# Kernel tuning notes

Hardware: AMD Instinct MI355X
Metric: run time of the kernel (lower is better)

## Reference

```python
import jax, jax.numpy as jnp
import numpy as np

H = 256          # hidden_size
HH, WW = 4, 4
CONV = HH * WW * H   # 4096, conv_out_size
N = 16           # n_subtasks
S = 32           # subtask_size
B = 256          # batch
T = 128          # timesteps
TOT = N + S + H + S + 1 + 1  # 338, RecurrentState width


def setup_inputs() -> dict:
    key = jax.random.key(0)
    ks = jax.random.split(key, 12)
    w = lambda k, shape: (jax.random.normal(k, shape) * 0.02).astype(jnp.float32)
    obs = jax.random.normal(ks[0], (T, B, CONV), jnp.float32)
    task = jax.random.normal(ks[1], (B, N, S), jnp.float32)
    hx0 = jnp.zeros((B, TOT), jnp.float32).at[:, :N].set(1.0 / N)  # uniform pointer init
    return dict(
        obs=obs, task=task, hx0=hx0,
        W_ih=w(ks[2], (3 * H, H)), W_hh=w(ks[3], (3 * H, H)),
        b_ih=jnp.zeros((3 * H,), jnp.float32), b_hh=jnp.zeros((3 * H,), jnp.float32),
        W_f=w(ks[4], (H, CONV + 2 * S + 1)), b_f=jnp.zeros((H,), jnp.float32),
        W_u=w(ks[5], (1, 2 * H)), b_u=jnp.zeros((1,), jnp.float32),
        W_s=w(ks[6], (3, H)), b_s=jnp.zeros((3,), jnp.float32),
        W_pi=w(ks[7], (N, H + S)), b_pi=jnp.zeros((N,), jnp.float32),
        W_beta=w(ks[8], (2, CONV + S)), b_beta=jnp.zeros((2,), jnp.float32),
    )


def reference(obs, task, hx0, W_ih, W_hh, b_ih, b_hh, W_f, b_f, W_u, b_u,
              W_s, b_s, W_pi, b_pi, W_beta, b_beta):
    M = task  # [B, N, S] subtask memory
    p0 = hx0[:, :N]
    r0 = hx0[:, N:N + S]
    h0 = hx0[:, N + S:N + S + H]
    g0 = hx0[:, N + S + H:N + S + H + S]
    b0 = hx0[:, N + S + H + S:N + S + H + S + 1]
    keys = jax.random.split(jax.random.key(42), T * 2).reshape(T, 2)

    def gru(x, h):  # torch.nn.GRUCell math
        gi = x @ W_ih.T + b_ih
        gh = h @ W_hh.T + b_hh
        ir, iz, inn = jnp.split(gi, 3, axis=-1)
        hr, hz, hn = jnp.split(gh, 3, axis=-1)
        rr = jax.nn.sigmoid(ir + hr)
        z = jax.nn.sigmoid(iz + hz)
        n = jnp.tanh(inn + rr * hn)
        return (1.0 - z) * n + z * h

    def step(carry, xs):
        p, r, h, b = carry[0], carry[1], carry[2], carry[4]
        g = carry[3]
        x, kk = xs
        # s = f(cat(x, r, g, b))
        s = jnp.concatenate([x, r, g, b], axis=-1) @ W_f.T + b_f
        # update gate c = sigmoid(phi_update(cat(s, h)))
        c = jax.nn.sigmoid(jnp.concatenate([s, h], axis=-1) @ W_u.T + b_u)  # [B,1]
        h_new = gru(s, h)
        # pointer shift: l = softmax(phi_shift(h_old)); p = conv1d(p, l) (same-pad, k=3)
        l = jax.nn.softmax(h @ W_s.T + b_s, axis=1)  # [B,3]
        pp = jnp.pad(p, ((0, 0), (1, 1)))
        p_new = l[:, 0:1] * pp[:, :N] + l[:, 1:2] * pp[:, 1:N + 1] + l[:, 2:3] * pp[:, 2:N + 2]
        # memory read r = p @ M
        r_new = jnp.einsum('bn,bns->bs', p_new, M)
        p = c * p_new + (1.0 - c) * p
        r = c * r_new + (1.0 - c) * r
        h = c * h_new + (1.0 - c) * h
        # sample g ~ Cat(pi_theta(h, r)); g embedding = selected memory row
        logits_g = jnp.concatenate([h, r], axis=-1) @ W_pi.T + b_pi  # [B,N]
        g_idx = jax.random.categorical(kk[0], logits_g)  # [B] int
        lp_g = jnp.take_along_axis(jax.nn.log_softmax(logits_g, axis=-1), g_idx[:, None], axis=1)  # [B,1]
        g_vec = jnp.take_along_axis(M, g_idx[:, None, None], axis=1)[:, 0, :]  # [B,S]
        g = c * g_vec + (1.0 - c) * g
        # sample b ~ Cat(beta(x, g))
        logits_b = jnp.concatenate([x, g], axis=-1) @ W_beta.T + b_beta  # [B,2]
        b_idx = jax.random.categorical(kk[1], logits_b)
        lp_b = jnp.take_along_axis(jax.nn.log_softmax(logits_b, axis=-1), b_idx[:, None], axis=1)
        b = b_idx[:, None].astype(jnp.float32)
        log_prob = lp_g + lp_b
        out = jnp.concatenate([p, r, h, g, b, log_prob], axis=-1)  # [B, TOT]
        return (p, r, h, g, b), out

    _, outs = jax.lax.scan(step, (p0, r0, h0, g0, b0), (obs, keys))
    return outs  # [T, B, TOT]
```

## Files before the change

kernel.cpp:

```cpp
#include <hip/hip_runtime.h>


#define RNG_PARTITIONABLE 1

#define T_STEPS 128
#define B_ROWS  256
#define TOT     338
#define CONV    4096
#define LDWF    4161
#define LDWB    4128

typedef float v2f __attribute__((ext_vector_type(2)));

__device__ __forceinline__ void tf2x32(unsigned k0, unsigned k1, unsigned c0, unsigned c1,
                                       unsigned &o0, unsigned &o1) {
  const unsigned ks2 = k0 ^ k1 ^ 0x1BD11BDAu;
  unsigned x0 = c0 + k0;
  unsigned x1 = c1 + k1;
#define TFR(r) { x0 += x1; x1 = (x1 << (r)) | (x1 >> (32 - (r))); x1 ^= x0; }
  TFR(13) TFR(15) TFR(26) TFR(6)
  x0 += k1; x1 += ks2 + 1u;
  TFR(17) TFR(29) TFR(16) TFR(24)
  x0 += ks2; x1 += k0 + 2u;
  TFR(13) TFR(15) TFR(26) TFR(6)
  x0 += k0; x1 += k1 + 3u;
  TFR(17) TFR(29) TFR(16) TFR(24)
  x0 += k1; x1 += ks2 + 4u;
  TFR(13) TFR(15) TFR(26) TFR(6)
  x0 += ks2; x1 += k0 + 5u;
#undef TFR
  o0 = x0; o1 = x1;
}

__device__ __forceinline__ void rng_key(unsigned j, unsigned &k0, unsigned &k1) {
#if RNG_PARTITIONABLE
  tf2x32(0u, 42u, 0u, j, k0, k1);
#else
  unsigned w[2];
  for (int q = 0; q < 2; ++q) {
    unsigned i = 2u*j + (unsigned)q, a, b;
    if (i < 256u) { tf2x32(0u, 42u, i, 256u + i, a, b); w[q] = a; }
    else          { tf2x32(0u, 42u, i - 256u, i, a, b); w[q] = b; }
  }
  k0 = w[0]; k1 = w[1];
#endif
}

__device__ __forceinline__ unsigned rng_bits(unsigned k0, unsigned k1, unsigned idx, unsigned total) {
#if RNG_PARTITIONABLE
  unsigned o0, o1;
  tf2x32(k0, k1, 0u, idx, o0, o1);
  return o0 ^ o1;
#else
  unsigned half = total >> 1, o0, o1;
  if (idx < half) { tf2x32(k0, k1, idx, half + idx, o0, o1); return o0; }
  else            { tf2x32(k0, k1, idx - half, idx, o0, o1); return o1; }
#endif
}

__device__ __forceinline__ float gumbel_from_bits(unsigned bits) {
  float u0 = __uint_as_float(0x3f800000u | (bits >> 9)) - 1.0f;
  float u  = fmaxf(u0, 1.17549435e-38f);
  return -logf(-logf(u));
}

__global__ __launch_bounds__(256) void rng_k(float* __restrict__ ggum, float* __restrict__ bgum) {
  unsigned tid = blockIdx.x * 256u + threadIdx.x;
  const unsigned NG = T_STEPS * B_ROWS * 16;
  const unsigned NB = T_STEPS * B_ROWS * 2;
  if (tid < NG) {
    unsigned t = tid / (B_ROWS * 16);
    unsigned i = tid % (B_ROWS * 16);
    unsigned k0, k1; rng_key(2u * t, k0, k1);
    ggum[tid] = gumbel_from_bits(rng_bits(k0, k1, i, B_ROWS * 16));
  } else if (tid < NG + NB) {
    unsigned q = tid - NG;
    unsigned t = q / (B_ROWS * 2);
    unsigned i = q % (B_ROWS * 2);
    unsigned k0, k1; rng_key(2u * t + 1u, k0, k1);
    bgum[q] = gumbel_from_bits(rng_bits(k0, k1, i, B_ROWS * 2));
  }
}

__global__ __launch_bounds__(768) void prep4_k(const float* __restrict__ W_ih,
                                               const float* __restrict__ W_hh,
                                               float4* __restrict__ WT4) {
  int k2 = blockIdx.x & 127;
  int copy = blockIdx.x >> 7;
  int col = threadIdx.x;
  float a0 = W_ih[(size_t)col * 256 + 2 * k2];
  float a1 = W_ih[(size_t)col * 256 + 2 * k2 + 1];
  float b0 = W_hh[(size_t)col * 256 + 2 * k2];
  float b1 = W_hh[(size_t)col * 256 + 2 * k2 + 1];
  WT4[(size_t)copy * 98304 + (size_t)k2 * 768 + col] = make_float4(a0, b0, a1, b1);
}

__device__ __forceinline__ float waveRed(float v) {
  v += __shfl_down(v, 32, 64);
  v += __shfl_down(v, 16, 64);
  v += __shfl_down(v, 8, 64);
  v += __shfl_down(v, 4, 64);
  v += __shfl_down(v, 2, 64);
  v += __shfl_down(v, 1, 64);
  return v;
}

__global__ __launch_bounds__(256) void bx_k(const float* __restrict__ obs,
                                            const float* __restrict__ W_beta,
                                            const float* __restrict__ b_beta,
                                            float* __restrict__ bxv) {
  int m = blockIdx.x, tid = threadIdx.x;
  const float* row = obs + (size_t)m * CONV;
  float p0 = 0.f, p1 = 0.f;
  for (int i = tid; i < CONV; i += 256) {
    float o = row[i];
    p0 = fmaf(o, W_beta[i], p0);
    p1 = fmaf(o, W_beta[LDWB + i], p1);
  }
  p0 = waveRed(p0); p1 = waveRed(p1);
  __shared__ float sc[2][4];
  int w = tid >> 6;
  if ((tid & 63) == 0) { sc[0][w] = p0; sc[1][w] = p1; }
  __syncthreads();
  if (tid == 0) bxv[(size_t)m * 2 + 0] = sc[0][0] + sc[0][1] + sc[0][2] + sc[0][3] + b_beta[0];
  if (tid == 1) bxv[(size_t)m * 2 + 1] = sc[1][0] + sc[1][1] + sc[1][2] + sc[1][3] + b_beta[1];
}

struct __attribute__((packed, aligned(4))) F4 { float x, y, z, w; };

__global__ __launch_bounds__(256) void gemm1_k(const float* __restrict__ A,
                                               const float* __restrict__ W,
                                               const float* __restrict__ bias,
                                               float* __restrict__ C1) {
  __shared__ __align__(16) float As[32][68];
  __shared__ __align__(16) float Bs[32][68];
  int bid = blockIdx.x;
  int mt = bid & 511, nt = bid >> 9;
  int m0 = mt * 64, n0 = nt * 64;
  int tid = threadIdx.x;
  int tm = tid & 15, tn = tid >> 4;
  int lr = tid >> 2;
  int lc = (tid & 3) * 8;
  v2f acc[4][2];
#pragma unroll
  for (int i = 0; i < 4; ++i) { acc[i][0] = (v2f){0.f, 0.f}; acc[i][1] = (v2f){0.f, 0.f}; }
  for (int k0 = 0; k0 < CONV; k0 += 32) {
    F4 a0 = *(const F4*)(A + (size_t)(m0 + lr) * CONV + k0 + lc);
    F4 a1 = *(const F4*)(A + (size_t)(m0 + lr) * CONV + k0 + lc + 4);
    F4 b0 = *(const F4*)(W + (size_t)(n0 + lr) * LDWF + k0 + lc);
    F4 b1 = *(const F4*)(W + (size_t)(n0 + lr) * LDWF + k0 + lc + 4);
    __syncthreads();
    As[lc + 0][lr] = a0.x; As[lc + 1][lr] = a0.y; As[lc + 2][lr] = a0.z; As[lc + 3][lr] = a0.w;
    As[lc + 4][lr] = a1.x; As[lc + 5][lr] = a1.y; As[lc + 6][lr] = a1.z; As[lc + 7][lr] = a1.w;
    Bs[lc + 0][lr] = b0.x; Bs[lc + 1][lr] = b0.y; Bs[lc + 2][lr] = b0.z; Bs[lc + 3][lr] = b0.w;
    Bs[lc + 4][lr] = b1.x; Bs[lc + 5][lr] = b1.y; Bs[lc + 6][lr] = b1.z; Bs[lc + 7][lr] = b1.w;
    __syncthreads();
#pragma unroll
    for (int kk = 0; kk < 32; ++kk) {
      const float4 av = *(const float4*)&As[kk][tm * 4];
      const float4 bv = *(const float4*)&Bs[kk][tn * 4];
      const v2f bl = (v2f){bv.x, bv.y};
      const v2f bh = (v2f){bv.z, bv.w};
      const float aa[4] = {av.x, av.y, av.z, av.w};
#pragma unroll
      for (int i = 0; i < 4; ++i) {
        v2f ax = (v2f){aa[i], aa[i]};
        acc[i][0] = __builtin_elementwise_fma(ax, bl, acc[i][0]);
        acc[i][1] = __builtin_elementwise_fma(ax, bh, acc[i][1]);
      }
    }
  }
  const int mrow = m0 + tm * 4;
  const int ncol = n0 + tn * 4;
  float4 bv4 = *(const float4*)(bias + ncol);
#pragma unroll
  for (int i = 0; i < 4; ++i) {
    float4 v;
    v.x = acc[i][0].x + bv4.x; v.y = acc[i][0].y + bv4.y;
    v.z = acc[i][1].x + bv4.z; v.w = acc[i][1].y + bv4.w;
    *(float4*)(C1 + (size_t)(mrow + i) * 256 + ncol) = v;
  }
}

__global__ __launch_bounds__(256, 1) void seq_k(
    const float* __restrict__ hx0, const float* __restrict__ task,
    const float* __restrict__ W_f, const float* __restrict__ WT4,
    const float* __restrict__ b_ih, const float* __restrict__ b_hh,
    const float* __restrict__ W_u, const float* __restrict__ b_u,
    const float* __restrict__ W_s, const float* __restrict__ b_s,
    const float* __restrict__ W_pi, const float* __restrict__ b_pi,
    const float* __restrict__ W_beta, const float* __restrict__ C1,
    const float* __restrict__ bxv, const float* __restrict__ ggum,
    const float* __restrict__ bgum, float* __restrict__ out) {
  const int b2 = blockIdx.x;
  const int tid = threadIdx.x;
  const int o = tid;
  const int brow0 = 2 * b2, brow1 = 2 * b2 + 1;
  const float4* __restrict__ wt = (const float4*)WT4 + (size_t)((b2 >> 3) & 1) * 98304;

  __shared__ float wf_sh[65 * 256];
  __shared__ float wpi_sh[288 * 16];
  __shared__ __align__(16) float4 SH4[2][2][128];
  __shared__ float M_sh[2][512];
  __shared__ float red4[2][4][4];
  __shared__ float red16[2][4][16];
  __shared__ float p_sh[2][2][16];
  __shared__ float r_sh[2][2][32];
  __shared__ float g_sh[2][2][32];
  __shared__ float gg_sh[2][16], bg_sh[2][2], bx_sh[2][2];
  __shared__ float wb_sh[2][32], bpi_sh[16];

  for (int i = tid; i < 65 * 256; i += 256) {
    int oo = i / 65, j = i % 65;
    wf_sh[i] = W_f[(size_t)oo * LDWF + CONV + j];
  }
  for (int i = tid; i < 288 * 16; i += 256) wpi_sh[i] = W_pi[i];
  float hold0 = hx0[brow0 * TOT + 48 + o];
  float hold1 = hx0[brow1 * TOT + 48 + o];
  if (tid < 16) {
    p_sh[0][0][tid] = hx0[brow0 * TOT + tid];
    p_sh[1][0][tid] = hx0[brow1 * TOT + tid];
  }
  if (tid < 32) {
    r_sh[0][0][tid] = hx0[brow0 * TOT + 16 + tid];
    r_sh[1][0][tid] = hx0[brow1 * TOT + 16 + tid];
    g_sh[0][0][tid] = hx0[brow0 * TOT + 304 + tid];
    g_sh[1][0][tid] = hx0[brow1 * TOT + 304 + tid];
    wb_sh[0][tid] = W_beta[CONV + tid];
    wb_sh[1][tid] = W_beta[LDWB + CONV + tid];
  }
  if (tid >= 32 && tid < 48) bpi_sh[tid - 32] = b_pi[tid - 32];
  M_sh[0][tid] = task[(size_t)brow0 * 512 + tid];
  M_sh[0][256 + tid] = task[(size_t)brow0 * 512 + 256 + tid];
  M_sh[1][tid] = task[(size_t)brow1 * 512 + tid];
  M_sh[1][256 + tid] = task[(size_t)brow1 * 512 + 256 + tid];
  float bnew0 = hx0[brow0 * TOT + 336];
  float bnew1 = hx0[brow1 * TOT + 336];

  const float bih_r = b_ih[o], bih_z = b_ih[256 + o], bih_n = b_ih[512 + o];
  const float bhh_r = b_hh[o], bhh_z = b_hh[256 + o], bhh_n = b_hh[512 + o];
  const float wu_s = W_u[o], wu_h = W_u[256 + o];
  const float ws0 = W_s[o], ws1 = W_s[256 + o], ws2 = W_s[512 + o];
  const float bu0 = b_u[0], bs0 = b_s[0], bs1 = b_s[1], bs2 = b_s[2];
  __syncthreads();

  float sacc0, sacc1;
  {
    const float* wfr = wf_sh + o * 65;
    sacc0 = C1[(size_t)brow0 * 256 + o];
    sacc1 = C1[(size_t)brow1 * 256 + o];
#pragma unroll
    for (int j = 0; j < 32; ++j) sacc0 = fmaf(r_sh[0][0][j], wfr[j], sacc0);
#pragma unroll
    for (int j = 0; j < 32; ++j) sacc0 = fmaf(g_sh[0][0][j], wfr[32 + j], sacc0);
    sacc0 = fmaf(bnew0, wfr[64], sacc0);
#pragma unroll
    for (int j = 0; j < 32; ++j) sacc1 = fmaf(r_sh[1][0][j], wfr[j], sacc1);
#pragma unroll
    for (int j = 0; j < 32; ++j) sacc1 = fmaf(g_sh[1][0][j], wfr[32 + j], sacc1);
    sacc1 = fmaf(bnew1, wfr[64], sacc1);
    ((float*)&SH4[0][0][o >> 1])[(o & 1) * 2]     = sacc0;
    ((float*)&SH4[0][0][o >> 1])[(o & 1) * 2 + 1] = hold0;
    ((float*)&SH4[0][1][o >> 1])[(o & 1) * 2]     = sacc1;
    ((float*)&SH4[0][1][o >> 1])[(o & 1) * 2 + 1] = hold1;
  }
  {
    float pc0 = fmaf(wu_s, sacc0, wu_h * hold0);
    float q00 = ws0 * hold0, q01 = ws1 * hold0, q02 = ws2 * hold0;
    float pc1 = fmaf(wu_s, sacc1, wu_h * hold1);
    float q10 = ws0 * hold1, q11 = ws1 * hold1, q12 = ws2 * hold1;
    pc0 = waveRed(pc0); q00 = waveRed(q00); q01 = waveRed(q01); q02 = waveRed(q02);
    pc1 = waveRed(pc1); q10 = waveRed(q10); q11 = waveRed(q11); q12 = waveRed(q12);
    int w4 = tid >> 6;
    if ((tid & 63) == 0) {
      red4[0][w4][0] = pc0; red4[0][w4][1] = q00; red4[0][w4][2] = q01; red4[0][w4][3] = q02;
      red4[1][w4][0] = pc1; red4[1][w4][1] = q10; red4[1][w4][2] = q11; red4[1][w4][3] = q12;
    }
  }
  __syncthreads();

  for (int t = 0; t < T_STEPS; ++t) {
    const int pp = t & 1, np = pp ^ 1;

    int tn2 = (t + 1 < T_STEPS) ? t + 1 : t;
    float c1n0 = C1[((size_t)tn2 * 256 + brow0) * 256 + o];
    float c1n1 = C1[((size_t)tn2 * 256 + brow1) * 256 + o];
    if (tid < 32) {
      int rr = tid >> 4, j = tid & 15;
      gg_sh[rr][j] = ggum[((size_t)t * 256 + brow0 + rr) * 16 + j];
    } else if (tid < 36) {
      int q = tid - 32;
      bg_sh[q >> 1][q & 1] = bgum[((size_t)t * 256 + brow0 + (q >> 1)) * 2 + (q & 1)];
    } else if (tid < 40) {
      int q = tid - 36;
      bx_sh[q >> 1][q & 1] = bxv[((size_t)t * 256 + brow0 + (q >> 1)) * 2 + (q & 1)];
    }

    v2f ar0 = (v2f){0.f, 0.f}, az0 = (v2f){0.f, 0.f}, an0 = (v2f){0.f, 0.f};
    v2f ar1 = (v2f){0.f, 0.f}, az1 = (v2f){0.f, 0.f}, an1 = (v2f){0.f, 0.f};
#pragma unroll 4
    for (int k2 = 0; k2 < 128; ++k2) {
      float4 wr = wt[(size_t)(k2 * 3 + 0) * 256 + o];
      float4 wz = wt[(size_t)(k2 * 3 + 1) * 256 + o];
      float4 wn = wt[(size_t)(k2 * 3 + 2) * 256 + o];
      float4 x0 = SH4[pp][0][k2];
      float4 x1 = SH4[pp][1][k2];
      v2f xa0 = (v2f){x0.x, x0.y}, xb0 = (v2f){x0.z, x0.w};
      v2f xa1 = (v2f){x1.x, x1.y}, xb1 = (v2f){x1.z, x1.w};
      ar0 = __builtin_elementwise_fma(xa0, (v2f){wr.x, wr.y}, ar0);
      ar0 = __builtin_elementwise_fma(xb0, (v2f){wr.z, wr.w}, ar0);
      az0 = __builtin_elementwise_fma(xa0, (v2f){wz.x, wz.y}, az0);
      az0 = __builtin_elementwise_fma(xb0, (v2f){wz.z, wz.w}, az0);
      an0 = __builtin_elementwise_fma(xa0, (v2f){wn.x, wn.y}, an0);
      an0 = __builtin_elementwise_fma(xb0, (v2f){wn.z, wn.w}, an0);
      ar1 = __builtin_elementwise_fma(xa1, (v2f){wr.x, wr.y}, ar1);
      ar1 = __builtin_elementwise_fma(xb1, (v2f){wr.z, wr.w}, ar1);
      az1 = __builtin_elementwise_fma(xa1, (v2f){wz.x, wz.y}, az1);
      az1 = __builtin_elementwise_fma(xb1, (v2f){wz.z, wz.w}, az1);
      an1 = __builtin_elementwise_fma(xa1, (v2f){wn.x, wn.y}, an1);
      an1 = __builtin_elementwise_fma(xb1, (v2f){wn.z, wn.w}, an1);
    }

    float c0, c1, l00, l01, l02, l10, l11, l12;
    {
      float cs0 = red4[0][0][0] + red4[0][1][0] + red4[0][2][0] + red4[0][3][0] + bu0;
      c0 = 1.0f / (1.0f + expf(-cs0));
      float x0 = red4[0][0][1] + red4[0][1][1] + red4[0][2][1] + red4[0][3][1] + bs0;
      float x1 = red4[0][0][2] + red4[0][1][2] + red4[0][2][2] + red4[0][3][2] + bs1;
      float x2 = red4[0][0][3] + red4[0][1][3] + red4[0][2][3] + red4[0][3][3] + bs2;
      float m = fmaxf(x0, fmaxf(x1, x2));
      float e0 = expf(x0 - m), e1 = expf(x1 - m), e2 = expf(x2 - m);
      float es = e0 + e1 + e2;
      l00 = e0 / es; l01 = e1 / es; l02 = e2 / es;
      float cs1 = red4[1][0][0] + red4[1][1][0] + red4[1][2][0] + red4[1][3][0] + bu0;
      c1 = 1.0f / (1.0f + expf(-cs1));
      float y0 = red4[1][0][1] + red4[1][1][1] + red4[1][2][1] + red4[1][3][1] + bs0;
      float y1 = red4[1][0][2] + red4[1][1][2] + red4[1][2][2] + red4[1][3][2] + bs1;
      float y2 = red4[1][0][3] + red4[1][1][3] + red4[1][2][3] + red4[1][3][3] + bs2;
      float mm = fmaxf(y0, fmaxf(y1, y2));
      float f0 = expf(y0 - mm), f1 = expf(y1 - mm), f2 = expf(y2 - mm);
      float fs = f0 + f1 + f2;
      l10 = f0 / fs; l11 = f1 / fs; l12 = f2 / fs;
    }
    const float omc0 = 1.0f - c0, omc1 = 1.0f - c1;

    float pn0[16], pn1[16];
#pragma unroll
    for (int i = 0; i < 16; ++i) {
      float pm0 = (i > 0) ? p_sh[0][pp][i - 1] : 0.f;
      float pq0 = (i < 15) ? p_sh[0][pp][i + 1] : 0.f;
      pn0[i] = l00 * pm0 + l01 * p_sh[0][pp][i] + l02 * pq0;
      float pm1 = (i > 0) ? p_sh[1][pp][i - 1] : 0.f;
      float pq1 = (i < 15) ? p_sh[1][pp][i + 1] : 0.f;
      pn1[i] = l10 * pm1 + l11 * p_sh[1][pp][i] + l12 * pq1;
    }
    float hg0, hg1;
    {
      float rr_ = 1.0f / (1.0f + expf(-(ar0.x + bih_r + ar0.y + bhh_r)));
      float zz = 1.0f / (1.0f + expf(-(az0.x + bih_z + az0.y + bhh_z)));
      float nn = tanhf(an0.x + bih_n + rr_ * (an0.y + bhh_n));
      float hnew = (1.0f - zz) * nn + zz * hold0;
      hg0 = c0 * hnew + omc0 * hold0;
      ((float*)&SH4[np][0][o >> 1])[(o & 1) * 2 + 1] = hg0;
      float rr1 = 1.0f / (1.0f + expf(-(ar1.x + bih_r + ar1.y + bhh_r)));
      float zz1 = 1.0f / (1.0f + expf(-(az1.x + bih_z + az1.y + bhh_z)));
      float nn1 = tanhf(an1.x + bih_n + rr1 * (an1.y + bhh_n));
      float hnew1 = (1.0f - zz1) * nn1 + zz1 * hold1;
      hg1 = c1 * hnew1 + omc1 * hold1;
      ((float*)&SH4[np][1][o >> 1])[(o & 1) * 2 + 1] = hg1;
    }
    float rv0 = 0.f, rv1 = 0.f;
    if (tid < 32) {
      float a0 = 0.f, a1 = 0.f;
#pragma unroll
      for (int n2 = 0; n2 < 16; ++n2) a0 = fmaf(pn0[n2], M_sh[0][n2 * 32 + o], a0);
#pragma unroll
      for (int n2 = 0; n2 < 16; ++n2) a1 = fmaf(pn1[n2], M_sh[1][n2 * 32 + o], a1);
      rv0 = c0 * a0 + omc0 * r_sh[0][pp][o];
      rv1 = c1 * a1 + omc1 * r_sh[1][pp][o];
      r_sh[0][np][o] = rv0;
      r_sh[1][np][o] = rv1;
    }
    if (tid < 16) {
      p_sh[0][np][o] = c0 * pn0[o] + omc0 * p_sh[0][pp][o];
      p_sh[1][np][o] = c1 * pn1[o] + omc1 * p_sh[1][pp][o];
    }
    {
      float pv0[16], pv1[16];
#pragma unroll
      for (int o2 = 0; o2 < 16; ++o2) {
        pv0[o2] = hg0 * wpi_sh[o2 * 288 + o];
        pv1[o2] = hg1 * wpi_sh[o2 * 288 + o];
      }
      if (tid < 32) {
#pragma unroll
        for (int o2 = 0; o2 < 16; ++o2) {
          pv0[o2] = fmaf(rv0, wpi_sh[o2 * 288 + 256 + o], pv0[o2]);
          pv1[o2] = fmaf(rv1, wpi_sh[o2 * 288 + 256 + o], pv1[o2]);
        }
      }
#pragma unroll
      for (int o2 = 0; o2 < 16; ++o2) { pv0[o2] = waveRed(pv0[o2]); pv1[o2] = waveRed(pv1[o2]); }
      int w4 = tid >> 6;
      if ((tid & 63) == 0) {
#pragma unroll
        for (int o2 = 0; o2 < 16; ++o2) { red16[0][w4][o2] = pv0[o2]; red16[1][w4][o2] = pv1[o2]; }
      }
    }
    hold0 = hg0; hold1 = hg1;
    __syncthreads();

    int gidx0 = 0, gidx1 = 0;
    float lpg0, lpg1;
    {
      float lg[16];
#pragma unroll
      for (int n2 = 0; n2 < 16; ++n2)
        lg[n2] = red16[0][0][n2] + red16[0][1][n2] + red16[0][2][n2] + red16[0][3][n2] + bpi_sh[n2];
      float best = -3.402823466e+38f;
      for (int n2 = 0; n2 < 16; ++n2) {
        float v = lg[n2] + gg_sh[0][n2];
        if (v > best) { best = v; gidx0 = n2; }
      }
      float mx = lg[0];
      for (int n2 = 1; n2 < 16; ++n2) mx = fmaxf(mx, lg[n2]);
      float se = 0.f;
      for (int n2 = 0; n2 < 16; ++n2) se += expf(lg[n2] - mx);
      lpg0 = lg[gidx0] - mx - logf(se);
      float best1 = -3.402823466e+38f;
#pragma unroll
      for (int n2 = 0; n2 < 16; ++n2)
        lg[n2] = red16[1][0][n2] + red16[1][1][n2] + red16[1][2][n2] + red16[1][3][n2] + bpi_sh[n2];
      for (int n2 = 0; n2 < 16; ++n2) {
        float v = lg[n2] + gg_sh[1][n2];
        if (v > best1) { best1 = v; gidx1 = n2; }
      }
      float mx1 = lg[0];
      for (int n2 = 1; n2 < 16; ++n2) mx1 = fmaxf(mx1, lg[n2]);
      float se1 = 0.f;
      for (int n2 = 0; n2 < 16; ++n2) se1 += expf(lg[n2] - mx1);
      lpg1 = lg[gidx1] - mx1 - logf(se1);
    }
    if (tid < 32) {
      g_sh[0][np][o] = c0 * M_sh[0][gidx0 * 32 + o] + omc0 * g_sh[0][pp][o];
      g_sh[1][np][o] = c1 * M_sh[1][gidx1 * 32 + o] + omc1 * g_sh[1][pp][o];
    }
    float lpt0, lpt1;
    {
      float lb0 = bx_sh[0][0], lb1 = bx_sh[0][1];
      for (int s2 = 0; s2 < 32; ++s2) {
        float gv = c0 * M_sh[0][gidx0 * 32 + s2] + omc0 * g_sh[0][pp][s2];
        lb0 = fmaf(gv, wb_sh[0][s2], lb0);
        lb1 = fmaf(gv, wb_sh[1][s2], lb1);
      }
      int bidx = ((lb1 + bg_sh[0][1]) > (lb0 + bg_sh[0][0])) ? 1 : 0;
      float mb = fmaxf(lb0, lb1);
      float seb = expf(lb0 - mb) + expf(lb1 - mb);
      bnew0 = (float)bidx;
      lpt0 = lpg0 + ((bidx ? lb1 : lb0) - mb - logf(seb));
      float mb1_0 = bx_sh[1][0], mb1_1 = bx_sh[1][1];
      for (int s2 = 0; s2 < 32; ++s2) {
        float gv = c1 * M_sh[1][gidx1 * 32 + s2] + omc1 * g_sh[1][pp][s2];
        mb1_0 = fmaf(gv, wb_sh[0][s2], mb1_0);
        mb1_1 = fmaf(gv, wb_sh[1][s2], mb1_1);
      }
      int bidx1 = ((mb1_1 + bg_sh[1][1]) > (mb1_0 + bg_sh[1][0])) ? 1 : 0;
      float mbm = fmaxf(mb1_0, mb1_1);
      float seb1 = expf(mb1_0 - mbm) + expf(mb1_1 - mbm);
      bnew1 = (float)bidx1;
      lpt1 = lpg1 + ((bidx1 ? mb1_1 : mb1_0) - mbm - logf(seb1));
    }
    {
      const float* wfr = wf_sh + o * 65;
      sacc0 = c1n0;
#pragma unroll
      for (int j = 0; j < 32; ++j) sacc0 = fmaf(r_sh[0][np][j], wfr[j], sacc0);
#pragma unroll
      for (int j = 0; j < 32; ++j) {
        float gv = c0 * M_sh[0][gidx0 * 32 + j] + omc0 * g_sh[0][pp][j];
        sacc0 = fmaf(gv, wfr[32 + j], sacc0);
      }
      sacc0 = fmaf(bnew0, wfr[64], sacc0);
      ((float*)&SH4[np][0][o >> 1])[(o & 1) * 2] = sacc0;
      sacc1 = c1n1;
#pragma unroll
      for (int j = 0; j < 32; ++j) sacc1 = fmaf(r_sh[1][np][j], wfr[j], sacc1);
#pragma unroll
      for (int j = 0; j < 32; ++j) {
        float gv = c1 * M_sh[1][gidx1 * 32 + j] + omc1 * g_sh[1][pp][j];
        sacc1 = fmaf(gv, wfr[32 + j], sacc1);
      }
      sacc1 = fmaf(bnew1, wfr[64], sacc1);
      ((float*)&SH4[np][1][o >> 1])[(o & 1) * 2] = sacc1;
    }
    {
      float pc0 = fmaf(wu_s, sacc0, wu_h * hold0);
      float q00 = ws0 * hold0, q01 = ws1 * hold0, q02 = ws2 * hold0;
      float pc1 = fmaf(wu_s, sacc1, wu_h * hold1);
      float q10 = ws0 * hold1, q11 = ws1 * hold1, q12 = ws2 * hold1;
      pc0 = waveRed(pc0); q00 = waveRed(q00); q01 = waveRed(q01); q02 = waveRed(q02);
      pc1 = waveRed(pc1); q10 = waveRed(q10); q11 = waveRed(q11); q12 = waveRed(q12);
      int w4 = tid >> 6;
      if ((tid & 63) == 0) {
        red4[0][w4][0] = pc0; red4[0][w4][1] = q00; red4[0][w4][2] = q01; red4[0][w4][3] = q02;
        red4[1][w4][0] = pc1; red4[1][w4][1] = q10; red4[1][w4][2] = q11; red4[1][w4][3] = q12;
      }
    }
    {
      size_t base0 = ((size_t)t * 256 + brow0) * TOT;
      size_t base1 = ((size_t)t * 256 + brow1) * TOT;
      out[base0 + 48 + o] = hg0;
      out[base1 + 48 + o] = hg1;
      if (tid < 16) {
        out[base0 + tid] = p_sh[0][np][tid];
        out[base1 + tid] = p_sh[1][np][tid];
      }
      if (tid < 32) {
        out[base0 + 16 + tid] = r_sh[0][np][tid];
        out[base1 + 16 + tid] = r_sh[1][np][tid];
        out[base0 + 304 + tid] = c0 * M_sh[0][gidx0 * 32 + tid] + omc0 * g_sh[0][pp][tid];
        out[base1 + 304 + tid] = c1 * M_sh[1][gidx1 * 32 + tid] + omc1 * g_sh[1][pp][tid];
      }
      if (tid == 32) { out[base0 + 336] = bnew0; out[base1 + 336] = bnew1; }
      if (tid == 33) { out[base0 + 337] = lpt0; out[base1 + 337] = lpt1; }
    }
    __syncthreads();
  }
}

extern "C" void kernel_launch(void* const* d_in, const int* in_sizes, int n_in,
                              void* d_out, int out_size, void* d_ws, size_t ws_size,
                              hipStream_t stream) {
  const float* obs    = (const float*)d_in[0];
  const float* task   = (const float*)d_in[1];
  const float* hx0    = (const float*)d_in[2];
  const float* W_ih   = (const float*)d_in[3];
  const float* W_hh   = (const float*)d_in[4];
  const float* b_ih   = (const float*)d_in[5];
  const float* b_hh   = (const float*)d_in[6];
  const float* W_f    = (const float*)d_in[7];
  const float* b_f    = (const float*)d_in[8];
  const float* W_u    = (const float*)d_in[9];
  const float* b_u    = (const float*)d_in[10];
  const float* W_s    = (const float*)d_in[11];
  const float* b_s    = (const float*)d_in[12];
  const float* W_pi   = (const float*)d_in[13];
  const float* b_pi   = (const float*)d_in[14];
  const float* W_beta = (const float*)d_in[15];
  const float* b_beta = (const float*)d_in[16];

  char* ws = (char*)d_ws;
  size_t off = 0;
  auto take = [&](size_t bytes) {
    size_t r = off;
    off += (bytes + 255) & ~(size_t)255;
    return r;
  };
  size_t off_WT4  = take((size_t)2 * 98304 * 16);
  size_t off_ggum = take((size_t)T_STEPS * B_ROWS * 16 * 4);
  size_t off_bgum = take((size_t)T_STEPS * B_ROWS * 2 * 4);
  size_t off_bx   = take((size_t)T_STEPS * B_ROWS * 2 * 4);
  size_t off_C1   = take((size_t)T_STEPS * B_ROWS * 256 * 4);
  if (off > ws_size) return;

  float* WT4  = (float*)(ws + off_WT4);
  float* ggum = (float*)(ws + off_ggum);
  float* bgum = (float*)(ws + off_bgum);
  float* bxv  = (float*)(ws + off_bx);
  float* C1   = (float*)(ws + off_C1);

  hipLaunchKernelGGL(prep4_k, dim3(256), dim3(768), 0, stream, W_ih, W_hh, (float4*)WT4);
  hipLaunchKernelGGL(rng_k, dim3(2304), dim3(256), 0, stream, ggum, bgum);
  hipLaunchKernelGGL(gemm1_k, dim3(2048), dim3(256), 0, stream, obs, W_f, b_f, C1);
  hipLaunchKernelGGL(bx_k, dim3(32768), dim3(256), 0, stream, obs, W_beta, b_beta, bxv);
  hipLaunchKernelGGL(seq_k, dim3(128), dim3(256), 0, stream,
                     hx0, task, W_f, WT4, b_ih, b_hh, W_u, b_u, W_s, b_s, W_pi, b_pi,
                     W_beta, C1, bxv, ggum, bgum, (float*)d_out);
}
```

Before: 3.998 ms.

## Pin part of GRU recurrent weights in registers/LDS and prefetch gemm tiles

In the sequential kernel, the first 16 k-slices of the recurrent weight tile are held in registers for the whole run and the next 4 are staged in shared memory. Only the remaining slices are streamed from global memory on each timestep, which cuts per-step global/L2 traffic. The tiled input GEMM also now loads the next K tile into registers while the current tile is being computed, a software-pipelining prefetch. The cost is about 192 extra VGPRs per thread plus 48KB more LDS, which risks spills or exceeding the LDS budget.

```diff
diff --git a/kernel.cpp b/kernel.cpp
--- a/kernel.cpp
+++ b/kernel.cpp
@@ -9,6 +9,9 @@
 #define CONV    4096
 #define LDWF    4161
 #define LDWB    4128
+
+#define NREG    16
+#define NLDS    4
 
 typedef float v2f __attribute__((ext_vector_type(2)));
 
@@ -144,17 +147,23 @@
   v2f acc[4][2];
 #pragma unroll
   for (int i = 0; i < 4; ++i) { acc[i][0] = (v2f){0.f, 0.f}; acc[i][1] = (v2f){0.f, 0.f}; }
+  F4 a0 = *(const F4*)(A + (size_t)(m0 + lr) * CONV + lc);
+  F4 a1 = *(const F4*)(A + (size_t)(m0 + lr) * CONV + lc + 4);
+  F4 b0 = *(const F4*)(W + (size_t)(n0 + lr) * LDWF + lc);
+  F4 b1 = *(const F4*)(W + (size_t)(n0 + lr) * LDWF + lc + 4);
   for (int k0 = 0; k0 < CONV; k0 += 32) {
-    F4 a0 = *(const F4*)(A + (size_t)(m0 + lr) * CONV + k0 + lc);
-    F4 a1 = *(const F4*)(A + (size_t)(m0 + lr) * CONV + k0 + lc + 4);
-    F4 b0 = *(const F4*)(W + (size_t)(n0 + lr) * LDWF + k0 + lc);
-    F4 b1 = *(const F4*)(W + (size_t)(n0 + lr) * LDWF + k0 + lc + 4);
     __syncthreads();
     As[lc + 0][lr] = a0.x; As[lc + 1][lr] = a0.y; As[lc + 2][lr] = a0.z; As[lc + 3][lr] = a0.w;
     As[lc + 4][lr] = a1.x; As[lc + 5][lr] = a1.y; As[lc + 6][lr] = a1.z; As[lc + 7][lr] = a1.w;
     Bs[lc + 0][lr] = b0.x; Bs[lc + 1][lr] = b0.y; Bs[lc + 2][lr] = b0.z; Bs[lc + 3][lr] = b0.w;
     Bs[lc + 4][lr] = b1.x; Bs[lc + 5][lr] = b1.y; Bs[lc + 6][lr] = b1.z; Bs[lc + 7][lr] = b1.w;
     __syncthreads();
+    if (k0 + 32 < CONV) {
+      a0 = *(const F4*)(A + (size_t)(m0 + lr) * CONV + k0 + 32 + lc);
+      a1 = *(const F4*)(A + (size_t)(m0 + lr) * CONV + k0 + 32 + lc + 4);
+      b0 = *(const F4*)(W + (size_t)(n0 + lr) * LDWF + k0 + 32 + lc);
+      b1 = *(const F4*)(W + (size_t)(n0 + lr) * LDWF + k0 + 32 + lc + 4);
+    }
 #pragma unroll
     for (int kk = 0; kk < 32; ++kk) {
       const float4 av = *(const float4*)&As[kk][tm * 4];
@@ -200,6 +209,7 @@
 
   __shared__ float wf_sh[65 * 256];
   __shared__ float wpi_sh[288 * 16];
+  __shared__ __align__(16) float4 wlds[NLDS][3][256];
   __shared__ __align__(16) float4 SH4[2][2][128];
   __shared__ float M_sh[2][512];
   __shared__ float red4[2][4][4];
@@ -215,6 +225,17 @@
     wf_sh[i] = W_f[(size_t)oo * LDWF + CONV + j];
   }
   for (int i = tid; i < 288 * 16; i += 256) wpi_sh[i] = W_pi[i];
+  for (int i = tid; i < NLDS * 3 * 256; i += 256) {
+    int g = i / 768, rem = i % 768;
+    wlds[g][rem >> 8][rem & 255] = wt[(size_t)((NREG + g) * 3 + (rem >> 8)) * 256 + (rem & 255)];
+  }
+  float4 wregr[NREG], wregz[NREG], wregn[NREG];
+#pragma unroll
+  for (int q = 0; q < NREG; ++q) {
+    wregr[q] = wt[(size_t)(q * 3 + 0) * 256 + o];
+    wregz[q] = wt[(size_t)(q * 3 + 1) * 256 + o];
+    wregn[q] = wt[(size_t)(q * 3 + 2) * 256 + o];
+  }
   float hold0 = hx0[brow0 * TOT + 48 + o];
   float hold1 = hx0[brow1 * TOT + 48 + o];
   if (tid < 16) {
@@ -298,28 +319,44 @@
 
     v2f ar0 = (v2f){0.f, 0.f}, az0 = (v2f){0.f, 0.f}, an0 = (v2f){0.f, 0.f};
     v2f ar1 = (v2f){0.f, 0.f}, az1 = (v2f){0.f, 0.f}, an1 = (v2f){0.f, 0.f};
+#define K2_BODY(WR, WZ, WN, K2IDX)                                             \
+    {                                                                          \
+      float4 x0 = SH4[pp][0][K2IDX];                                           \
+      float4 x1 = SH4[pp][1][K2IDX];                                           \
+      v2f xa0 = (v2f){x0.x, x0.y}, xb0 = (v2f){x0.z, x0.w};                    \
+      v2f xa1 = (v2f){x1.x, x1.y}, xb1 = (v2f){x1.z, x1.w};                    \
+      ar0 = __builtin_elementwise_fma(xa0, (v2f){WR.x, WR.y}, ar0);            \
+      ar0 = __builtin_elementwise_fma(xb0, (v2f){WR.z, WR.w}, ar0);            \
+      az0 = __builtin_elementwise_fma(xa0, (v2f){WZ.x, WZ.y}, az0);            \
+      az0 = __builtin_elementwise_fma(xb0, (v2f){WZ.z, WZ.w}, az0);            \
+      an0 = __builtin_elementwise_fma(xa0, (v2f){WN.x, WN.y}, an0);            \
+      an0 = __builtin_elementwise_fma(xb0, (v2f){WN.z, WN.w}, an0);            \
+      ar1 = __builtin_elementwise_fma(xa1, (v2f){WR.x, WR.y}, ar1);            \
+      ar1 = __builtin_elementwise_fma(xb1, (v2f){WR.z, WR.w}, ar1);            \
+      az1 = __builtin_elementwise_fma(xa1, (v2f){WZ.x, WZ.y}, az1);            \
+      az1 = __builtin_elementwise_fma(xb1, (v2f){WZ.z, WZ.w}, az1);            \
+      an1 = __builtin_elementwise_fma(xa1, (v2f){WN.x, WN.y}, an1);            \
+      an1 = __builtin_elementwise_fma(xb1, (v2f){WN.z, WN.w}, an1);            \
+    }
+#pragma unroll
+    for (int q = 0; q < NREG; ++q) {
+      K2_BODY(wregr[q], wregz[q], wregn[q], q)
+    }
+#pragma unroll
+    for (int q = 0; q < NLDS; ++q) {
+      float4 wr = wlds[q][0][o];
+      float4 wz = wlds[q][1][o];
+      float4 wn = wlds[q][2][o];
+      K2_BODY(wr, wz, wn, (NREG + q))
+    }
 #pragma unroll 4
-    for (int k2 = 0; k2 < 128; ++k2) {
+    for (int k2 = NREG + NLDS; k2 < 128; ++k2) {
       float4 wr = wt[(size_t)(k2 * 3 + 0) * 256 + o];
       float4 wz = wt[(size_t)(k2 * 3 + 1) * 256 + o];
       float4 wn = wt[(size_t)(k2 * 3 + 2) * 256 + o];
-      float4 x0 = SH4[pp][0][k2];
-      float4 x1 = SH4[pp][1][k2];
-      v2f xa0 = (v2f){x0.x, x0.y}, xb0 = (v2f){x0.z, x0.w};
-      v2f xa1 = (v2f){x1.x, x1.y}, xb1 = (v2f){x1.z, x1.w};
-      ar0 = __builtin_elementwise_fma(xa0, (v2f){wr.x, wr.y}, ar0);
-      ar0 = __builtin_elementwise_fma(xb0, (v2f){wr.z, wr.w}, ar0);
-      az0 = __builtin_elementwise_fma(xa0, (v2f){wz.x, wz.y}, az0);
-      az0 = __builtin_elementwise_fma(xb0, (v2f){wz.z, wz.w}, az0);
-      an0 = __builtin_elementwise_fma(xa0, (v2f){wn.x, wn.y}, an0);
-      an0 = __builtin_elementwise_fma(xb0, (v2f){wn.z, wn.w}, an0);
-      ar1 = __builtin_elementwise_fma(xa1, (v2f){wr.x, wr.y}, ar1);
-      ar1 = __builtin_elementwise_fma(xb1, (v2f){wr.z, wr.w}, ar1);
-      az1 = __builtin_elementwise_fma(xa1, (v2f){wz.x, wz.y}, az1);
-      az1 = __builtin_elementwise_fma(xb1, (v2f){wz.z, wz.w}, az1);
-      an1 = __builtin_elementwise_fma(xa1, (v2f){wn.x, wn.y}, an1);
-      an1 = __builtin_elementwise_fma(xb1, (v2f){wn.z, wn.w}, an1);
-    }
+      K2_BODY(wr, wz, wn, k2)
+    }
+#undef K2_BODY
 
     float c0, c1, l00, l01, l02, l10, l11, l12;
     {
```

Measured after the change: 4.997 ms. 25.0% more time.
